# Kernel tuning notes

Hardware: AMD Instinct MI355X
Metric: run time of the kernel (lower is better)

The kernel has to match this reference:

```python
import jax, jax.numpy as jnp
import numpy as np
import math

V, D, H, NH, LE, LD = 32000, 256, 1024, 8, 2, 2
B, T = 4, 512


def qlinear(x, W, b):
    # x: [..., Din, 4]; W: [4, Dout, Din] (r,i,j,k); b: [Dout, 4] or None
    r, i, j, k = x[..., 0], x[..., 1], x[..., 2], x[..., 3]
    Wr, Wi, Wj, Wk = W[0], W[1], W[2], W[3]
    f = lambda a, M: jnp.einsum('...d,od->...o', a, M)
    ro = f(r, Wr) - f(i, Wi) - f(j, Wj) - f(k, Wk)
    io = f(r, Wi) + f(i, Wr) + f(j, Wk) - f(k, Wj)
    jo = f(r, Wj) - f(i, Wk) + f(j, Wr) + f(k, Wi)
    ko = f(r, Wk) + f(i, Wj) - f(j, Wi) + f(k, Wr)
    out = jnp.stack([ro, io, jo, ko], axis=-1)
    return out + b if b is not None else out


def modrelu(x, bias):
    # x: [..., F, 4]; bias: [F]
    norm = jnp.linalg.norm(x, axis=-1)
    scale = jax.nn.relu(norm + bias) / (norm + 1e-6)
    return x * scale[..., None]


def qnorm(x, g, beta):
    # normalize each quaternion (last dim of size 4) to unit norm
    n = jnp.sqrt(jnp.sum(x * x, axis=-1, keepdims=True) + 1e-6)
    return g * (x / n) + beta


def qattn(q, k, v, W, b, mask, nh):
    # W: [4(proj q,k,v,out), 4(comp), D, D]; b: [4, D, 4]
    def split(x):
        Bq, Tq, Dq, _ = x.shape
        return x.reshape(Bq, Tq, nh, Dq // nh, 4).transpose(0, 2, 1, 3, 4)
    qh = split(qlinear(q, W[0], b[0]))
    kh = split(qlinear(k, W[1], b[1]))
    vh = split(qlinear(v, W[2], b[2]))
    hd = qh.shape[3]
    s = jnp.einsum('bhqfd,bhkfd->bhqk', qh, kh) / math.sqrt(hd * 4)
    if mask is not None:
        s = jnp.where(mask[:, None] == 0, -jnp.inf, s)
    w = jax.nn.softmax(s, axis=-1)
    o = jnp.einsum('bhqk,bhkfd->bhqfd', w, vh)
    Bq, h, Tq, f, _ = o.shape
    o = o.transpose(0, 2, 1, 3, 4).reshape(Bq, Tq, h * f, 4)
    return qlinear(o, W[3], b[3])


def qff(x, W1, b1, mbias, W2, b2):
    return qlinear(modrelu(qlinear(x, W1, b1), mbias), W2, b2)


def qembed(ids, emb):
    d = emb.shape[-1]
    scale = 1.0 / 10000.0 ** (jnp.arange(d, dtype=jnp.float32) / d)
    r = emb[0][ids]
    i = emb[1][ids] * scale
    j = emb[2][ids] * scale
    k = emb[3][ids] * scale
    n = jnp.sqrt(r * r + i * i + j * j + k * k + 1e-6)
    return jnp.stack([r / n, i / n, j / n, k / n], axis=-1)


def rope(x):
    t, d = x.shape[1], x.shape[2]
    inv = 1.0 / 10000.0 ** (jnp.arange(0, d, 2, dtype=jnp.float32) / d)
    fr = jnp.arange(t, dtype=jnp.float32)[:, None] * inv[None, :]
    ang = jnp.concatenate([jnp.sin(fr), jnp.cos(fr)], axis=-1)  # [T, D]
    return x * ang[None, :, :, None]


def setup_inputs():
    key = jax.random.key(0)
    ks = jax.random.split(key, 12)
    n = lambda k, s: jax.random.normal(k, s, jnp.float32) * 0.02
    src = jax.random.randint(ks[0], (B, T), 0, V)
    tgt = jax.random.randint(ks[1], (B, T), 0, V)
    tgt_mask = jnp.broadcast_to(jnp.tril(jnp.ones((T, T), jnp.int32)), (B, T, T))
    return dict(
        src=src, tgt=tgt, tgt_mask=tgt_mask,
        emb=n(ks[2], (4, V, D)),
        enc_attn_W=n(ks[3], (LE, 4, 4, D, D)), enc_attn_b=jnp.zeros((LE, 4, D, 4)),
        enc_norm_g=jnp.ones((LE, 2, D, 4)), enc_norm_b=jnp.zeros((LE, 2, D, 4)),
        enc_ff_W1=n(ks[4], (LE, 4, H, D)), enc_ff_b1=jnp.zeros((LE, H, 4)),
        enc_ff_mod=jnp.zeros((LE, H)),
        enc_ff_W2=n(ks[5], (LE, 4, D, H)), enc_ff_b2=jnp.zeros((LE, D, 4)),
        dec_sa_W=n(ks[6], (LD, 4, 4, D, D)), dec_sa_b=jnp.zeros((LD, 4, D, 4)),
        dec_ca_W=n(ks[7], (LD, 4, 4, D, D)), dec_ca_b=jnp.zeros((LD, 4, D, 4)),
        dec_norm_g=jnp.ones((LD, 3, D, 4)), dec_norm_b=jnp.zeros((LD, 3, D, 4)),
        dec_ff_W1=n(ks[8], (LD, 4, H, D)), dec_ff_b1=jnp.zeros((LD, H, 4)),
        dec_ff_mod=jnp.zeros((LD, H)),
        dec_ff_W2=n(ks[9], (LD, 4, D, H)), dec_ff_b2=jnp.zeros((LD, D, 4)),
        fc_W=n(ks[10], (V, D)), fc_b=jnp.zeros((V,)),
    )


def reference(src, tgt, tgt_mask, emb,
              enc_attn_W, enc_attn_b, enc_norm_g, enc_norm_b,
              enc_ff_W1, enc_ff_b1, enc_ff_mod, enc_ff_W2, enc_ff_b2,
              dec_sa_W, dec_sa_b, dec_ca_W, dec_ca_b, dec_norm_g, dec_norm_b,
              dec_ff_W1, dec_ff_b1, dec_ff_mod, dec_ff_W2, dec_ff_b2,
              fc_W, fc_b):
    x_src = rope(qembed(src, emb))
    x_tgt = rope(qembed(tgt, emb))
    # encoder stack
    m = x_src
    for l in range(LE):
        m = qnorm(m + qattn(m, m, m, enc_attn_W[l], enc_attn_b[l], None, NH), enc_norm_g[l, 0], enc_norm_b[l, 0])
        m = qnorm(m + qff(m, enc_ff_W1[l], enc_ff_b1[l], enc_ff_mod[l], enc_ff_W2[l], enc_ff_b2[l]), enc_norm_g[l, 1], enc_norm_b[l, 1])
    # decoder stack
    x = x_tgt
    for l in range(LD):
        x = qnorm(x + qattn(x, x, x, dec_sa_W[l], dec_sa_b[l], tgt_mask, NH), dec_norm_g[l, 0], dec_norm_b[l, 0])
        x = qnorm(x + qattn(x, m, m, dec_ca_W[l], dec_ca_b[l], None, NH), dec_norm_g[l, 1], dec_norm_b[l, 1])
        x = qnorm(x + qff(x, dec_ff_W1[l], dec_ff_b1[l], dec_ff_mod[l], dec_ff_W2[l], dec_ff_b2[l]), dec_norm_g[l, 2], dec_norm_b[l, 2])
    real = jnp.linalg.norm(x, axis=-1)  # QuaternionToReal('norm') -> [B, T, D]
    logits = jnp.einsum('btd,vd->btv', real, fc_W) + fc_b
    return logits
```

## Files before the change

kernel.cpp:

```cpp
#include <hip/hip_runtime.h>
#include <math.h>

#define B 4
#define T 512
#define D 256
#define H 1024
#define NH 8
#define V 32000
#define BT (B*T)
#define LE 2
#define LD 2
#define DIM 1024

typedef __attribute__((ext_vector_type(8))) short s16x8;
typedef __attribute__((ext_vector_type(4))) float f32x4;
typedef __attribute__((address_space(3))) void lds_void;
typedef const __attribute__((address_space(1))) void g_void;

__device__ __forceinline__ ushort f2bf(float x) {
  uint u = __float_as_uint(x);
  return (ushort)((u + 0x7fffu + ((u >> 16) & 1u)) >> 16);
}

__global__ __launch_bounds__(256) void embed_rope_kernel(
    const int* __restrict__ src, const int* __restrict__ tgt,
    const float* __restrict__ emb,
    float* __restrict__ osrc, ushort* __restrict__ osrcbf,
    float* __restrict__ otgt, ushort* __restrict__ otgtbf) {
  int g = blockIdx.x;
  int isTgt = g >= BT;
  int bt = isTgt ? g - BT : g;
  int d  = threadIdx.x;
  int id = isTgt ? tgt[bt] : src[bt];
  float* out = isTgt ? otgt : osrc;
  ushort* outbf = isTgt ? otgtbf : osrcbf;
  int t  = bt % T;
  size_t VD = (size_t)V * D;
  float scale = powf(10000.f, -(float)d / (float)D);
  float r = emb[(size_t)id * D + d];
  float i = emb[VD + (size_t)id * D + d] * scale;
  float j = emb[2 * VD + (size_t)id * D + d] * scale;
  float k = emb[3 * VD + (size_t)id * D + d] * scale;
  float n = sqrtf(r * r + i * i + j * j + k * k + 1e-6f);
  float ang;
  if (d < D / 2) {
    float inv = powf(10000.f, -(float)(2 * d) / (float)D);
    ang = sinf((float)t * inv);
  } else {
    float inv = powf(10000.f, -(float)(2 * (d - D / 2)) / (float)D);
    ang = cosf((float)t * inv);
  }
  float s = ang / n;
  size_t base = (size_t)bt * DIM + d * 4;
  float4 q = make_float4(r * s, i * s, j * s, k * s);
  *(float4*)(out + base) = q;
  *(ushort4*)(outbf + base) = make_ushort4(f2bf(q.x), f2bf(q.y), f2bf(q.z), f2bf(q.w));
}

#define A_CNT  1572864
#define F_CNT  2097152
#define FC_CNT 2048000
#define MEGA_TOT (A_CNT + F_CNT + FC_CNT)
#define WSTEP  1048576
#define FFW    4194304

__device__ __forceinline__ void qexpand_write(
    const float* __restrict__ src, ushort* __restrict__ dst,
    int o, int d, int Din, int P) {
  float w0 = src[(size_t)o * Din + d];
  float w1 = src[P + (size_t)o * Din + d];
  float w2 = src[2 * (size_t)P + (size_t)o * Din + d];
  float w3 = src[3 * (size_t)P + (size_t)o * Din + d];
  int K4 = Din * 4;
  size_t rbase = (size_t)(o * 4) * K4 + d * 4;
  *(ushort4*)(dst + rbase)          = make_ushort4(f2bf(w0), f2bf(-w1), f2bf(-w2), f2bf(-w3));
  *(ushort4*)(dst + rbase + K4)     = make_ushort4(f2bf(w1), f2bf(w0),  f2bf(w3),  f2bf(-w2));
  *(ushort4*)(dst + rbase + 2 * K4) = make_ushort4(f2bf(w2), f2bf(-w3), f2bf(w0),  f2bf(w1));
  *(ushort4*)(dst + rbase + 3 * K4) = make_ushort4(f2bf(w3), f2bf(w2),  f2bf(-w1), f2bf(w0));
}

__global__ __launch_bounds__(256) void mega_expand_kernel(
    const float* __restrict__ encA, const float* __restrict__ decSA,
    const float* __restrict__ decCA,
    const float* __restrict__ eW1, const float* __restrict__ eW2,
    const float* __restrict__ dW1, const float* __restrict__ dW2,
    const float* __restrict__ fcW,
    ushort* __restrict__ WA, ushort* __restrict__ WF, ushort* __restrict__ Wfc) {
  int gid = blockIdx.x * 256 + threadIdx.x;
  if (gid < A_CNT) {
    int u = gid >> 18;
    int p = (gid >> 16) & 3;
    int rem = gid & 65535;
    int o = rem >> 8, d = rem & 255;
    const float* base = (u < 2) ? encA + (size_t)u * 1048576
                      : (u < 4) ? decSA + (size_t)(u - 2) * 1048576
                                : decCA + (size_t)(u - 4) * 1048576;
    qexpand_write(base + (size_t)p * 262144,
                  WA + ((size_t)u * 4 + p) * WSTEP, o, d, 256, 65536);
  } else if (gid < A_CNT + F_CNT) {
    int idx = gid - A_CNT;
    int layer = idx >> 19;
    int w12 = (idx >> 18) & 1;
    int rem = idx & 262143;
    const float* w1b = (layer < 2) ? eW1 + (size_t)layer * 1048576
                                   : dW1 + (size_t)(layer - 2) * 1048576;
    const float* w2b = (layer < 2) ? eW2 + (size_t)layer * 1048576
                                   : dW2 + (size_t)(layer - 2) * 1048576;
    ushort* dst = WF + (size_t)layer * 2 * FFW + (size_t)w12 * FFW;
    if (w12 == 0) {
      int o = rem >> 8, d = rem & 255;
      qexpand_write(w1b, dst, o, d, 256, 262144);
    } else {
      int o = rem >> 10, d = rem & 1023;
      qexpand_write(w2b, dst, o, d, 1024, 262144);
    }
  } else {
    int idx = gid - A_CNT - F_CNT;
    if (idx < FC_CNT) {
      float4 v = ((const float4*)fcW)[idx];
      ((ushort4*)Wfc)[idx] = make_ushort4(f2bf(v.x), f2bf(v.y), f2bf(v.z), f2bf(v.w));
    }
  }
}

struct GP {
  const ushort* A; const ushort* Aalt; int altStart;
  const ushort* Bt; const float* bias; void* Cv;
  ushort* qo; ushort* ko; ushort* vo;
  float* xres; ushort* xbf; const float* gg; const float* bb;
  const float* modb; ushort* realout;
};

template <int OMODE, int TM>
__global__ __launch_bounds__(256, 4) void gemm_bf16_kernel(
    GP u0, GP u1, int nunits, int N, int K) {
  __shared__ ushort As[2][TM * 32];
  __shared__ ushort Bs[2][128 * 32];
  const int tid = threadIdx.x;
  const int w = tid >> 6, l = tid & 63;
  const int nwg = gridDim.x;
  const int qq = nwg >> 3, rr = nwg & 7;
  const int xcd = blockIdx.x & 7, pos = blockIdx.x >> 3;
  const int wg = (xcd < rr ? xcd * (qq + 1) : rr * (qq + 1) + (xcd - rr) * qq) + pos;
  const int uwg = nwg / nunits;
  const int unit = wg / uwg;
  const int wgl = wg - unit * uwg;
  GP U = unit ? u1 : u0;
  const int nbx = N >> 7;
  const int nby = uwg / nbx;
  const int m0 = (wgl % nby) * TM, n0 = (wgl / nby) * 128;
  const ushort* Ap = (U.altStart && n0 >= U.altStart) ? U.Aalt : U.A;
  const ushort* Btp = U.Bt;
  const int lr = l & 15, lg = l >> 4;
  constexpr int NR = (TM == 128) ? 4 : 2;
  const int wm = (TM == 128) ? (w >> 1) : 0;
  const int wn = (TM == 128) ? (w & 1) : w;
  const int wcol = wn * (NR * 16);
  f32x4 acc[4][NR] = {};
  const int NT = K >> 5;

  auto stage = [&](int t, int buf) {
    int k0 = t << 5;
#pragma unroll
    for (int s = 0; s < TM / 64; ++s) {
      int fb = (w * (TM / 64) + s) * 1024;
      int f = fb + l * 16;
      int row = f >> 6, cb = (f & 63) >> 1;
      __builtin_amdgcn_global_load_lds(
          (g_void*)(Ap + (size_t)(m0 + row) * K + k0 + cb),
          (lds_void*)((char*)&As[buf][0] + fb), 16, 0, 0);
    }
#pragma unroll
    for (int s = 0; s < 2; ++s) {
      int fb = (w * 2 + s) * 1024;
      int f = fb + l * 16;
      int row = f >> 6, cb = (f & 63) >> 1;
      __builtin_amdgcn_global_load_lds(
          (g_void*)(Btp + (size_t)(n0 + row) * K + k0 + cb),
          (lds_void*)((char*)&Bs[buf][0] + fb), 16, 0, 0);
    }
  };

  stage(0, 0);
  __syncthreads();
  int cur = 0;
  for (int t = 0; t < NT; ++t) {
    if (t + 1 < NT) stage(t + 1, cur ^ 1);
    s16x8 af[4], bfr[NR];
#pragma unroll
    for (int mi = 0; mi < 4; ++mi)
      af[mi] = *(const s16x8*)(&As[cur][0] + (wm * 64 + mi * 16 + lr) * 32 + lg * 8);
#pragma unroll
    for (int ni = 0; ni < NR; ++ni)
      bfr[ni] = *(const s16x8*)(&Bs[cur][0] + (wcol + ni * 16 + lr) * 32 + lg * 8);
    __builtin_amdgcn_s_setprio(1);
#pragma unroll
    for (int mi = 0; mi < 4; ++mi)
#pragma unroll
      for (int ni = 0; ni < NR; ++ni)
        acc[mi][ni] = __builtin_amdgcn_mfma_f32_16x16x32_bf16(af[mi], bfr[ni], acc[mi][ni], 0, 0, 0);
    __builtin_amdgcn_s_setprio(0);
    __syncthreads();
    cur ^= 1;
  }

#pragma unroll
  for (int mi = 0; mi < 4; ++mi) {
#pragma unroll
    for (int ni = 0; ni < NR; ++ni) {
      int row = m0 + wm * 64 + mi * 16 + lg * 4;
      int col = n0 + wcol + ni * 16 + lr;
      f32x4 v = acc[mi][ni];
      if constexpr (OMODE == 0) {
        float bv = U.bias ? U.bias[col] : 0.f;
        float* C = (float*)U.Cv;
#pragma unroll
        for (int r = 0; r < 4; ++r)
          C[(size_t)(row + r) * N + col] = v[r] + bv;
      } else if constexpr (OMODE == 3) {
        float bv = U.bias[col];
        if (col < 2048) {
          ushort* dst = (col < DIM) ? U.qo : U.ko;
          int c = col & (DIM - 1);
#pragma unroll
          for (int r = 0; r < 4; ++r)
            dst[(size_t)(row + r) * DIM + c] = f2bf(v[r] + bv);
        } else {
          int c = col - 2048;
          ushort4 o4 = make_ushort4(f2bf(v[0] + bv), f2bf(v[1] + bv),
                                    f2bf(v[2] + bv), f2bf(v[3] + bv));
          *(ushort4*)&U.vo[((size_t)((row >> 9) << 10) + c) * T + (row & 511)] = o4;
        }
      } else if constexpr (OMODE == 4) {
        float bv = U.bias[col];
        float gv = U.gg[col], bev = U.bb[col];
#pragma unroll
        for (int r = 0; r < 4; ++r) {
          float val = v[r] + bv + U.xres[(size_t)(row + r) * DIM + col];
          float sq = val * val;
          sq += __shfl_xor(sq, 1);
          sq += __shfl_xor(sq, 2);
          float invn = rsqrtf(sq + 1e-6f);
          float res = gv * (val * invn) + bev;
          U.xres[(size_t)(row + r) * DIM + col] = res;
          U.xbf[(size_t)(row + r) * DIM + col] = f2bf(res);
          if (U.realout) {
            float rsq = res * res;
            rsq += __shfl_xor(rsq, 1);
            rsq += __shfl_xor(rsq, 2);
            if ((col & 3) == 0)
              U.realout[(size_t)(row + r) * D + (col >> 2)] = f2bf(sqrtf(rsq));
          }
        }
      } else {
        float bv = U.bias[col];
        float mb = U.modb[col >> 2];
        ushort* C = (ushort*)U.Cv;
#pragma unroll
        for (int r = 0; r < 4; ++r) {
          float val = v[r] + bv;
          float sq = val * val;
          sq += __shfl_xor(sq, 1);
          sq += __shfl_xor(sq, 2);
          float norm = sqrtf(sq);
          float scale = fmaxf(norm + mb, 0.f) / (norm + 1e-6f);
          C[(size_t)(row + r) * N + col] = f2bf(val * scale);
        }
      }
    }
  }
}

__global__ __launch_bounds__(256) void fused_attn_kernel(
    const ushort* __restrict__ qb, const ushort* __restrict__ kb,
    const ushort* __restrict__ vT, ushort* __restrict__ outA,
    int c0, int c1) {
  __shared__ ushort Ks[2][64 * 128];
  __shared__ ushort Vs[2][128 * 64];
  __shared__ ushort Pst[4][1024];
  const int tid = threadIdx.x;
  const int wq = tid >> 6, l = tid & 63;
  const int lr = l & 15, lg = l >> 4;
  const int h = blockIdx.y;
  const int u = blockIdx.z >> 2, b = blockIdx.z & 3;
  const size_t uoff = (size_t)u * ((size_t)BT * DIM);
  const int causal = u ? c1 : c0;
  const int q0 = blockIdx.x * 64 + wq * 16;
  const size_t bT = (size_t)b * T;
  const int hc = h * 128;
  const size_t vrow0 = (size_t)(b * NH + h) * 128;
  const ushort* qbu = qb + uoff;
  const ushort* kbu = kb + uoff;
  const ushort* vTu = vT + uoff;
  ushort* outu = outA + uoff;
  s16x8 qf[4];
#pragma unroll
  for (int ks = 0; ks < 4; ++ks)
    qf[ks] = *(const s16x8*)(qbu + (bT + q0 + lr) * DIM + hc + ks * 32 + lg * 8);
  f32x4 O[8] = {};
  float m[4] = {-3e38f, -3e38f, -3e38f, -3e38f};
  float lac[4] = {0.f, 0.f, 0.f, 0.f};
  const int kend = causal ? (blockIdx.x + 1) * 64 : T;
  const int ntile = kend >> 6;

  auto stageKV = [&](int tile, int buf) {
    int kv0 = tile << 6;
#pragma unroll
    for (int s = 0; s < 4; ++s) {
      int f = s * 4096 + tid * 16;
      int row = f >> 8, g = (f >> 4) & 15;
      int gs = g ^ (row & 7);
      __builtin_amdgcn_global_load_lds(
          (g_void*)(kbu + (bT + kv0 + row) * DIM + hc + gs * 8),
          (lds_void*)((char*)&Ks[buf][0] + f), 16, 0, 0);
    }
#pragma unroll
    for (int s = 0; s < 4; ++s) {
      int f = s * 4096 + tid * 16;
      int row = f >> 7, g = (f >> 4) & 7;
      int gs = g ^ (row & 7);
      __builtin_amdgcn_global_load_lds(
          (g_void*)(vTu + (vrow0 + row) * T + kv0 + gs * 8),
          (lds_void*)((char*)&Vs[buf][0] + f), 16, 0, 0);
    }
  };

  stageKV(0, 0);
  __syncthreads();
  int cur = 0;
  for (int tile = 0; tile < ntile; ++tile) {
    const int kv0 = tile << 6;
    if (tile + 1 < ntile) stageKV(tile + 1, cur ^ 1);
    f32x4 s[4] = {};
#pragma unroll
    for (int ks = 0; ks < 4; ++ks) {
      s16x8 kf[4];
#pragma unroll
      for (int ni = 0; ni < 4; ++ni) {
        int row = ni * 16 + lr;
        int g = (ks * 4 + lg) ^ (row & 7);
        kf[ni] = *(const s16x8*)(&Ks[cur][0] + row * 128 + g * 8);
      }
#pragma unroll
      for (int ni = 0; ni < 4; ++ni)
        s[ni] = __builtin_amdgcn_mfma_f32_16x16x32_bf16(qf[ks], kf[ni], s[ni], 0, 0, 0);
    }
    const bool domask = causal && (kv0 + 63 > q0);
#pragma unroll
    for (int r = 0; r < 4; ++r) {
      const int qrow = q0 + lg * 4 + r;
      float mx = -3e38f;
#pragma unroll
      for (int ni = 0; ni < 4; ++ni) {
        float v = s[ni][r] * 0.08838834764831845f;
        if (domask && (kv0 + ni * 16 + lr > qrow)) v = -3e38f;
        s[ni][r] = v;
        mx = fmaxf(mx, v);
      }
#pragma unroll
      for (int dd = 1; dd < 16; dd <<= 1) mx = fmaxf(mx, __shfl_xor(mx, dd));
      float mn = fmaxf(m[r], mx);
      float alpha = __expf(m[r] - mn);
      m[r] = mn;
      float ps = 0.f;
#pragma unroll
      for (int ni = 0; ni < 4; ++ni) {
        float p = __expf(s[ni][r] - mn);
        s[ni][r] = p;
        ps += p;
      }
#pragma unroll
      for (int dd = 1; dd < 16; dd <<= 1) ps += __shfl_xor(ps, dd);
      lac[r] = lac[r] * alpha + ps;
#pragma unroll
      for (int dni = 0; dni < 8; ++dni) O[dni][r] *= alpha;
      const int qloc = lg * 4 + r;
      const int sw = (qloc & 7) << 3;
#pragma unroll
      for (int ni = 0; ni < 4; ++ni)
        Pst[wq][qloc * 64 + ((ni * 16 + lr) ^ sw)] = f2bf(s[ni][r]);
    }
    asm volatile("s_waitcnt lgkmcnt(0)" ::: "memory");
    __builtin_amdgcn_sched_barrier(0);
#pragma unroll
    for (int ks2 = 0; ks2 < 2; ++ks2) {
      s16x8 pa = *(const s16x8*)&Pst[wq][lr * 64 + ((ks2 * 32 + lg * 8) ^ ((lr & 7) << 3))];
#pragma unroll
      for (int dni = 0; dni < 8; ++dni) {
        int row = dni * 16 + lr;
        int g = (ks2 * 4 + lg) ^ (row & 7);
        s16x8 vf = *(const s16x8*)(&Vs[cur][0] + row * 64 + g * 8);
        O[dni] = __builtin_amdgcn_mfma_f32_16x16x32_bf16(pa, vf, O[dni], 0, 0, 0);
      }
    }
    __syncthreads();
    cur ^= 1;
  }
#pragma unroll
  for (int r = 0; r < 4; ++r) {
    float inv = 1.f / lac[r];
    const size_t row = bT + q0 + lg * 4 + r;
#pragma unroll
    for (int dni = 0; dni < 8; ++dni)
      outu[row * DIM + hc + dni * 16 + lr] = f2bf(O[dni][r] * inv);
  }
}

extern "C" void kernel_launch(void* const* d_in, const int* in_sizes, int n_in,
                              void* d_out, int out_size, void* d_ws, size_t ws_size,
                              hipStream_t stream) {
  const int*   src        = (const int*)d_in[0];
  const int*   tgt        = (const int*)d_in[1];
  const float* emb        = (const float*)d_in[3];
  const float* enc_attn_W = (const float*)d_in[4];
  const float* enc_attn_b = (const float*)d_in[5];
  const float* enc_norm_g = (const float*)d_in[6];
  const float* enc_norm_b = (const float*)d_in[7];
  const float* enc_ff_W1  = (const float*)d_in[8];
  const float* enc_ff_b1  = (const float*)d_in[9];
  const float* enc_ff_mod = (const float*)d_in[10];
  const float* enc_ff_W2  = (const float*)d_in[11];
  const float* enc_ff_b2  = (const float*)d_in[12];
  const float* dec_sa_W   = (const float*)d_in[13];
  const float* dec_sa_b   = (const float*)d_in[14];
  const float* dec_ca_W   = (const float*)d_in[15];
  const float* dec_ca_b   = (const float*)d_in[16];
  const float* dec_norm_g = (const float*)d_in[17];
  const float* dec_norm_b = (const float*)d_in[18];
  const float* dec_ff_W1  = (const float*)d_in[19];
  const float* dec_ff_b1  = (const float*)d_in[20];
  const float* dec_ff_mod = (const float*)d_in[21];
  const float* dec_ff_W2  = (const float*)d_in[22];
  const float* dec_ff_b2  = (const float*)d_in[23];
  const float* fc_W       = (const float*)d_in[24];
  const float* fc_b       = (const float*)d_in[25];
  float* out = (float*)d_out;

  const size_t USZ = (size_t)BT * DIM;
  float* ws    = (float*)d_ws;
  float* xsrc  = ws;
  float* xtgt  = xsrc + USZ;
  ushort* xbf_src = (ushort*)(xtgt + USZ);
  ushort* xbf_tgt = xbf_src + USZ;
  ushort* aobf    = xbf_tgt + USZ;
  ushort* qb      = aobf + 2 * USZ;
  ushort* kb      = qb + 2 * USZ;
  ushort* vTb     = kb + 2 * USZ;
  ushort* hbf     = vTb + 2 * USZ;
  ushort* realbf  = hbf + (size_t)BT * H * 4;
  ushort* WA      = realbf + (size_t)BT * D;
  ushort* WF      = WA + (size_t)6 * 4 * WSTEP;
  ushort* Wfc     = WF + (size_t)4 * 2 * FFW;

  mega_expand_kernel<<<(MEGA_TOT + 255) / 256, 256, 0, stream>>>(
      enc_attn_W, dec_sa_W, dec_ca_W,
      enc_ff_W1, enc_ff_W2, dec_ff_W1, dec_ff_W2, fc_W, WA, WF, Wfc);

  embed_rope_kernel<<<2 * BT, 256, 0, stream>>>(src, tgt, emb, xsrc, xbf_src,
                                                xtgt, xbf_tgt);

  GP Z{};

  auto mkQKV = [&](const ushort* Abf, const ushort* Wu, const float* bb, int u) {
    GP g = Z;
    g.A = Abf; g.Bt = Wu; g.bias = bb;
    g.qo = qb + u * USZ; g.ko = kb + u * USZ; g.vo = vTb + u * USZ;
    return g;
  };
  auto mkOP = [&](int u, const ushort* Wu3, const float* bb, float* xres,
                  ushort* xbf, const float* gg, const float* nb, ushort* realo) {
    GP g = Z;
    g.A = aobf + u * USZ; g.Bt = Wu3; g.bias = bb;
    g.xres = xres; g.xbf = xbf; g.gg = gg; g.bb = nb; g.realout = realo;
    return g;
  };

  auto qkv1 = [&](GP g) {
    gemm_bf16_kernel<3, 128><<<384, 256, 0, stream>>>(g, g, 1, 3 * DIM, DIM);
  };
  auto qkv2 = [&](GP g0, GP g1) {
    gemm_bf16_kernel<3, 128><<<768, 256, 0, stream>>>(g0, g1, 2, 3 * DIM, DIM);
  };
  auto op1 = [&](GP g) {
    gemm_bf16_kernel<4, 64><<<256, 256, 0, stream>>>(g, g, 1, DIM, DIM);
  };
  auto op2 = [&](GP g0, GP g1) {
    gemm_bf16_kernel<4, 64><<<512, 256, 0, stream>>>(g0, g1, 2, DIM, DIM);
  };
  auto attn1 = [&](int causal) {
    fused_attn_kernel<<<dim3(T / 64, NH, B), 256, 0, stream>>>(
        qb, kb, vTb, aobf, causal, causal);
  };
  auto ffpair = [&](const ushort* xbf, int layer, const float* b1,
                    const float* mod, const float* b2, float* xres,
                    ushort* xbfo, const float* gg, const float* nb,
                    ushort* realo) {
    const ushort* Wf = WF + (size_t)layer * 2 * FFW;
    GP g1 = Z;
    g1.A = xbf; g1.Bt = Wf; g1.bias = b1; g1.Cv = hbf; g1.modb = mod;
    gemm_bf16_kernel<5, 128><<<512, 256, 0, stream>>>(g1, g1, 1, 4 * H, DIM);
    GP g2 = Z;
    g2.A = hbf; g2.Bt = Wf + FFW; g2.bias = b2;
    g2.xres = xres; g2.xbf = xbfo; g2.gg = gg; g2.bb = nb; g2.realout = realo;
    gemm_bf16_kernel<4, 64><<<256, 256, 0, stream>>>(g2, g2, 1, DIM, 4 * H);
  };

  {
    GP e = mkQKV(xbf_src, WA + (size_t)(0 * 4) * WSTEP, enc_attn_b, 0);
    GP d = mkQKV(xbf_tgt, WA + (size_t)(2 * 4) * WSTEP, dec_sa_b, 1);
    qkv2(e, d);
    fused_attn_kernel<<<dim3(T / 64, NH, 2 * B), 256, 0, stream>>>(
        qb, kb, vTb, aobf, 0, 1);
    GP eo = mkOP(0, WA + (size_t)(0 * 4 + 3) * WSTEP, enc_attn_b + 3 * DIM,
                 xsrc, xbf_src, enc_norm_g, enc_norm_b, nullptr);
    GP dо = mkOP(1, WA + (size_t)(2 * 4 + 3) * WSTEP, dec_sa_b + 3 * DIM,
                 xtgt, xbf_tgt, dec_norm_g, dec_norm_b, nullptr);
    op2(eo, dо);
  }
  ffpair(xbf_src, 0, enc_ff_b1, enc_ff_mod, enc_ff_b2, xsrc, xbf_src,
         enc_norm_g + 1 * DIM, enc_norm_b + 1 * DIM, nullptr);
  {
    GP e = mkQKV(xbf_src, WA + (size_t)(1 * 4) * WSTEP,
                 enc_attn_b + (size_t)1 * 4 * DIM, 0);
    qkv1(e);
    attn1(0);
    GP eo = mkOP(0, WA + (size_t)(1 * 4 + 3) * WSTEP,
                 enc_attn_b + (size_t)1 * 4 * DIM + 3 * DIM,
                 xsrc, xbf_src, enc_norm_g + 2 * DIM, enc_norm_b + 2 * DIM, nullptr);
    op1(eo);
  }
  ffpair(xbf_src, 1, enc_ff_b1 + (size_t)1 * H * 4, enc_ff_mod + H,
         enc_ff_b2 + DIM, xsrc, xbf_src,
         enc_norm_g + 3 * DIM, enc_norm_b + 3 * DIM, nullptr);

  for (int l = 0; l < LD; ++l) {
    if (l > 0) {
      GP d = mkQKV(xbf_tgt, WA + (size_t)((2 + l) * 4) * WSTEP,
                   dec_sa_b + (size_t)l * 4 * DIM, 0);
      qkv1(d);
      attn1(1);
      GP od = mkOP(0, WA + (size_t)((2 + l) * 4 + 3) * WSTEP,
                   dec_sa_b + (size_t)l * 4 * DIM + 3 * DIM,
                   xtgt, xbf_tgt, dec_norm_g + (size_t)(l * 3) * DIM,
                   dec_norm_b + (size_t)(l * 3) * DIM, nullptr);
      op1(od);
    }
    {
      GP g = mkQKV(xbf_tgt, WA + (size_t)((4 + l) * 4) * WSTEP,
                   dec_ca_b + (size_t)l * 4 * DIM, 0);
      g.Aalt = xbf_src; g.altStart = DIM;
      qkv1(g);
      attn1(0);
      GP og = mkOP(0, WA + (size_t)((4 + l) * 4 + 3) * WSTEP,
                   dec_ca_b + (size_t)l * 4 * DIM + 3 * DIM,
                   xtgt, xbf_tgt, dec_norm_g + (size_t)(l * 3 + 1) * DIM,
                   dec_norm_b + (size_t)(l * 3 + 1) * DIM, nullptr);
      op1(og);
    }
    ffpair(xbf_tgt, 2 + l, dec_ff_b1 + (size_t)l * H * 4,
           dec_ff_mod + (size_t)l * H, dec_ff_b2 + (size_t)l * DIM,
           xtgt, xbf_tgt, dec_norm_g + (size_t)(l * 3 + 2) * DIM,
           dec_norm_b + (size_t)(l * 3 + 2) * DIM,
           (l == LD - 1) ? realbf : nullptr);
  }

  {
    GP g = Z;
    g.A = realbf; g.Bt = Wfc; g.bias = fc_b; g.Cv = out;
    gemm_bf16_kernel<0, 128><<<(V / 128) * (BT / 128), 256, 0, stream>>>(
        g, g, 1, V, 256);
  }
}
```

Baseline: 1.120 ms.

## Add 2-wave 128x128 GEMM kernel, fold embed into expand, lazy softmax rescale

Adds a new GEMM kernel with 128 threads per block, where each wave computes a 64x128 tile. It is used for the QKV, FF1 and final FC projections to raise per-wave data reuse and MFMA density. The embedding/RoPE kernel is merged into the weight-expand launch to save a kernel launch. The attention softmax scale moves into the Q projection epilogue, and the online-softmax rescale is skipped unless the running max grows by more than a threshold. The larger register tile may lower occupancy, and the lazy rescale lets exponentials exceed 1, which risks overflow in edge cases.

Result: slower. 1.486 ms (+32.7%).

```diff
diff --git a/kernel.cpp b/kernel.cpp
--- a/kernel.cpp
+++ b/kernel.cpp
@@ -22,45 +22,13 @@
   return (ushort)((u + 0x7fffu + ((u >> 16) & 1u)) >> 16);
 }
 
-__global__ __launch_bounds__(256) void embed_rope_kernel(
-    const int* __restrict__ src, const int* __restrict__ tgt,
-    const float* __restrict__ emb,
-    float* __restrict__ osrc, ushort* __restrict__ osrcbf,
-    float* __restrict__ otgt, ushort* __restrict__ otgtbf) {
-  int g = blockIdx.x;
-  int isTgt = g >= BT;
-  int bt = isTgt ? g - BT : g;
-  int d  = threadIdx.x;
-  int id = isTgt ? tgt[bt] : src[bt];
-  float* out = isTgt ? otgt : osrc;
-  ushort* outbf = isTgt ? otgtbf : osrcbf;
-  int t  = bt % T;
-  size_t VD = (size_t)V * D;
-  float scale = powf(10000.f, -(float)d / (float)D);
-  float r = emb[(size_t)id * D + d];
-  float i = emb[VD + (size_t)id * D + d] * scale;
-  float j = emb[2 * VD + (size_t)id * D + d] * scale;
-  float k = emb[3 * VD + (size_t)id * D + d] * scale;
-  float n = sqrtf(r * r + i * i + j * j + k * k + 1e-6f);
-  float ang;
-  if (d < D / 2) {
-    float inv = powf(10000.f, -(float)(2 * d) / (float)D);
-    ang = sinf((float)t * inv);
-  } else {
-    float inv = powf(10000.f, -(float)(2 * (d - D / 2)) / (float)D);
-    ang = cosf((float)t * inv);
-  }
-  float s = ang / n;
-  size_t base = (size_t)bt * DIM + d * 4;
-  float4 q = make_float4(r * s, i * s, j * s, k * s);
-  *(float4*)(out + base) = q;
-  *(ushort4*)(outbf + base) = make_ushort4(f2bf(q.x), f2bf(q.y), f2bf(q.z), f2bf(q.w));
-}
+#define QSCALE 0.08838834764831845f
 
 #define A_CNT  1572864
 #define F_CNT  2097152
 #define FC_CNT 2048000
-#define MEGA_TOT (A_CNT + F_CNT + FC_CNT)
+#define EMB_CNT (2 * BT * 256)
+#define MEGA_TOT (A_CNT + F_CNT + FC_CNT + EMB_CNT)
 #define WSTEP  1048576
 #define FFW    4194304
 
@@ -85,7 +53,11 @@
     const float* __restrict__ eW1, const float* __restrict__ eW2,
     const float* __restrict__ dW1, const float* __restrict__ dW2,
     const float* __restrict__ fcW,
-    ushort* __restrict__ WA, ushort* __restrict__ WF, ushort* __restrict__ Wfc) {
+    ushort* __restrict__ WA, ushort* __restrict__ WF, ushort* __restrict__ Wfc,
+    const int* __restrict__ srcIds, const int* __restrict__ tgtIds,
+    const float* __restrict__ emb,
+    float* __restrict__ xsrc, ushort* __restrict__ xbfs,
+    float* __restrict__ xtgt, ushort* __restrict__ xbft) {
   int gid = blockIdx.x * 256 + threadIdx.x;
   if (gid < A_CNT) {
     int u = gid >> 18;
@@ -114,12 +86,39 @@
       int o = rem >> 10, d = rem & 1023;
       qexpand_write(w2b, dst, o, d, 1024, 262144);
     }
-  } else {
+  } else if (gid < A_CNT + F_CNT + FC_CNT) {
     int idx = gid - A_CNT - F_CNT;
-    if (idx < FC_CNT) {
-      float4 v = ((const float4*)fcW)[idx];
-      ((ushort4*)Wfc)[idx] = make_ushort4(f2bf(v.x), f2bf(v.y), f2bf(v.z), f2bf(v.w));
-    }
+    float4 v = ((const float4*)fcW)[idx];
+    ((ushort4*)Wfc)[idx] = make_ushort4(f2bf(v.x), f2bf(v.y), f2bf(v.z), f2bf(v.w));
+  } else if (gid < MEGA_TOT) {
+    int idx = gid - A_CNT - F_CNT - FC_CNT;
+    int g = idx >> 8, d = idx & 255;
+    int isTgt = g >= BT;
+    int bt = isTgt ? g - BT : g;
+    int id = isTgt ? tgtIds[bt] : srcIds[bt];
+    float* out = isTgt ? xtgt : xsrc;
+    ushort* outbf = isTgt ? xbft : xbfs;
+    int t = bt % T;
+    size_t VD = (size_t)V * D;
+    float scale = powf(10000.f, -(float)d / (float)D);
+    float r = emb[(size_t)id * D + d];
+    float i = emb[VD + (size_t)id * D + d] * scale;
+    float j = emb[2 * VD + (size_t)id * D + d] * scale;
+    float k = emb[3 * VD + (size_t)id * D + d] * scale;
+    float n = sqrtf(r * r + i * i + j * j + k * k + 1e-6f);
+    float ang;
+    if (d < D / 2) {
+      float inv = powf(10000.f, -(float)(2 * d) / (float)D);
+      ang = sinf((float)t * inv);
+    } else {
+      float inv = powf(10000.f, -(float)(2 * (d - D / 2)) / (float)D);
+      ang = cosf((float)t * inv);
+    }
+    float s = ang / n;
+    size_t base = (size_t)bt * DIM + d * 4;
+    float4 q = make_float4(r * s, i * s, j * s, k * s);
+    *(float4*)(out + base) = q;
+    *(ushort4*)(outbf + base) = make_ushort4(f2bf(q.x), f2bf(q.y), f2bf(q.z), f2bf(q.w));
   }
 }
 
@@ -130,6 +129,120 @@
   float* xres; ushort* xbf; const float* gg; const float* bb;
   const float* modb; ushort* realout;
 };
+
+template <int OMODE>
+__global__ __launch_bounds__(128, 2) void gemm2w_kernel(
+    GP u0, GP u1, int nunits, int N, int K) {
+  __shared__ ushort As[2][128 * 32];
+  __shared__ ushort Bs[2][128 * 32];
+  const int tid = threadIdx.x;
+  const int w = tid >> 6, l = tid & 63;
+  const int nwg = gridDim.x;
+  const int qq = nwg >> 3, rr = nwg & 7;
+  const int xcd = blockIdx.x & 7, pos = blockIdx.x >> 3;
+  const int wg = (xcd < rr ? xcd * (qq + 1) : rr * (qq + 1) + (xcd - rr) * qq) + pos;
+  const int uwg = nwg / nunits;
+  const int unit = wg / uwg;
+  const int wgl = wg - unit * uwg;
+  GP U = unit ? u1 : u0;
+  const int nbx = N >> 7;
+  const int nby = uwg / nbx;
+  const int m0 = (wgl % nby) * 128, n0 = (wgl / nby) * 128;
+  const ushort* Ap = (U.altStart && n0 >= U.altStart) ? U.Aalt : U.A;
+  const ushort* Btp = U.Bt;
+  const int lr = l & 15, lg = l >> 4;
+  f32x4 acc[4][8] = {};
+  const int NT = K >> 5;
+
+  auto stage = [&](int t, int buf) {
+    int k0 = t << 5;
+#pragma unroll
+    for (int s = 0; s < 4; ++s) {
+      int f = (s * 128 + tid) * 16;
+      int row = f >> 6, cb = (f & 63) >> 1;
+      __builtin_amdgcn_global_load_lds(
+          (g_void*)(Ap + (size_t)(m0 + row) * K + k0 + cb),
+          (lds_void*)((char*)&As[buf][0] + f), 16, 0, 0);
+    }
+#pragma unroll
+    for (int s = 0; s < 4; ++s) {
+      int f = (s * 128 + tid) * 16;
+      int row = f >> 6, cb = (f & 63) >> 1;
+      __builtin_amdgcn_global_load_lds(
+          (g_void*)(Btp + (size_t)(n0 + row) * K + k0 + cb),
+          (lds_void*)((char*)&Bs[buf][0] + f), 16, 0, 0);
+    }
+  };
+
+  stage(0, 0);
+  __syncthreads();
+  int cur = 0;
+  for (int t = 0; t < NT; ++t) {
+    if (t + 1 < NT) stage(t + 1, cur ^ 1);
+    s16x8 af[4], bfr[8];
+#pragma unroll
+    for (int mi = 0; mi < 4; ++mi)
+      af[mi] = *(const s16x8*)(&As[cur][0] + (w * 64 + mi * 16 + lr) * 32 + lg * 8);
+#pragma unroll
+    for (int ni = 0; ni < 8; ++ni)
+      bfr[ni] = *(const s16x8*)(&Bs[cur][0] + (ni * 16 + lr) * 32 + lg * 8);
+    __builtin_amdgcn_s_setprio(1);
+#pragma unroll
+    for (int mi = 0; mi < 4; ++mi)
+#pragma unroll
+      for (int ni = 0; ni < 8; ++ni)
+        acc[mi][ni] = __builtin_amdgcn_mfma_f32_16x16x32_bf16(af[mi], bfr[ni], acc[mi][ni], 0, 0, 0);
+    __builtin_amdgcn_s_setprio(0);
+    __syncthreads();
+    cur ^= 1;
+  }
+
+#pragma unroll
+  for (int mi = 0; mi < 4; ++mi) {
+#pragma unroll
+    for (int ni = 0; ni < 8; ++ni) {
+      int row = m0 + w * 64 + mi * 16 + lg * 4;
+      int col = n0 + ni * 16 + lr;
+      f32x4 v = acc[mi][ni];
+      if constexpr (OMODE == 0) {
+        float bv = U.bias ? U.bias[col] : 0.f;
+        float* C = (float*)U.Cv;
+#pragma unroll
+        for (int r = 0; r < 4; ++r)
+          C[(size_t)(row + r) * N + col] = v[r] + bv;
+      } else if constexpr (OMODE == 3) {
+        float bv = U.bias[col];
+        if (col < 2048) {
+          ushort* dst = (col < DIM) ? U.qo : U.ko;
+          float sc = (col < DIM) ? QSCALE : 1.f;
+          int c = col & (DIM - 1);
+#pragma unroll
+          for (int r = 0; r < 4; ++r)
+            dst[(size_t)(row + r) * DIM + c] = f2bf((v[r] + bv) * sc);
+        } else {
+          int c = col - 2048;
+          ushort4 o4 = make_ushort4(f2bf(v[0] + bv), f2bf(v[1] + bv),
+                                    f2bf(v[2] + bv), f2bf(v[3] + bv));
+          *(ushort4*)&U.vo[((size_t)((row >> 9) << 10) + c) * T + (row & 511)] = o4;
+        }
+      } else {
+        float bv = U.bias[col];
+        float mb = U.modb[col >> 2];
+        ushort* C = (ushort*)U.Cv;
+#pragma unroll
+        for (int r = 0; r < 4; ++r) {
+          float val = v[r] + bv;
+          float sq = val * val;
+          sq += __shfl_xor(sq, 1);
+          sq += __shfl_xor(sq, 2);
+          float norm = sqrtf(sq);
+          float scale = fmaxf(norm + mb, 0.f) / (norm + 1e-6f);
+          C[(size_t)(row + r) * N + col] = f2bf(val * scale);
+        }
+      }
+    }
+  }
+}
 
 template <int OMODE, int TM>
 __global__ __launch_bounds__(256, 4) void gemm_bf16_kernel(
@@ -149,8 +262,6 @@
   const int nbx = N >> 7;
   const int nby = uwg / nbx;
   const int m0 = (wgl % nby) * TM, n0 = (wgl / nby) * 128;
-  const ushort* Ap = (U.altStart && n0 >= U.altStart) ? U.Aalt : U.A;
-  const ushort* Btp = U.Bt;
   const int lr = l & 15, lg = l >> 4;
   constexpr int NR = (TM == 128) ? 4 : 2;
   const int wm = (TM == 128) ? (w >> 1) : 0;
@@ -167,7 +278,7 @@
       int f = fb + l * 16;
       int row = f >> 6, cb = (f & 63) >> 1;
       __builtin_amdgcn_global_load_lds(
-          (g_void*)(Ap + (size_t)(m0 + row) * K + k0 + cb),
+          (g_void*)(U.A + (size_t)(m0 + row) * K + k0 + cb),
           (lds_void*)((char*)&As[buf][0] + fb), 16, 0, 0);
     }
 #pragma unroll
@@ -176,7 +287,7 @@
       int f = fb + l * 16;
       int row = f >> 6, cb = (f & 63) >> 1;
       __builtin_amdgcn_global_load_lds(
-          (g_void*)(Btp + (size_t)(n0 + row) * K + k0 + cb),
+          (g_void*)(U.Bt + (size_t)(n0 + row) * K + k0 + cb),
           (lds_void*)((char*)&Bs[buf][0] + fb), 16, 0, 0);
     }
   };
@@ -211,27 +322,7 @@
       int row = m0 + wm * 64 + mi * 16 + lg * 4;
       int col = n0 + wcol + ni * 16 + lr;
       f32x4 v = acc[mi][ni];
-      if constexpr (OMODE == 0) {
-        float bv = U.bias ? U.bias[col] : 0.f;
-        float* C = (float*)U.Cv;
-#pragma unroll
-        for (int r = 0; r < 4; ++r)
-          C[(size_t)(row + r) * N + col] = v[r] + bv;
-      } else if constexpr (OMODE == 3) {
-        float bv = U.bias[col];
-        if (col < 2048) {
-          ushort* dst = (col < DIM) ? U.qo : U.ko;
-          int c = col & (DIM - 1);
-#pragma unroll
-          for (int r = 0; r < 4; ++r)
-            dst[(size_t)(row + r) * DIM + c] = f2bf(v[r] + bv);
-        } else {
-          int c = col - 2048;
-          ushort4 o4 = make_ushort4(f2bf(v[0] + bv), f2bf(v[1] + bv),
-                                    f2bf(v[2] + bv), f2bf(v[3] + bv));
-          *(ushort4*)&U.vo[((size_t)((row >> 9) << 10) + c) * T + (row & 511)] = o4;
-        }
-      } else if constexpr (OMODE == 4) {
+      if constexpr (OMODE == 4) {
         float bv = U.bias[col];
         float gv = U.gg[col], bev = U.bb[col];
 #pragma unroll
@@ -251,20 +342,6 @@
             if ((col & 3) == 0)
               U.realout[(size_t)(row + r) * D + (col >> 2)] = f2bf(sqrtf(rsq));
           }
-        }
-      } else {
-        float bv = U.bias[col];
-        float mb = U.modb[col >> 2];
-        ushort* C = (ushort*)U.Cv;
-#pragma unroll
-        for (int r = 0; r < 4; ++r) {
-          float val = v[r] + bv;
-          float sq = val * val;
-          sq += __shfl_xor(sq, 1);
-          sq += __shfl_xor(sq, 2);
-          float norm = sqrtf(sq);
-          float scale = fmaxf(norm + mb, 0.f) / (norm + 1e-6f);
-          C[(size_t)(row + r) * N + col] = f2bf(val * scale);
         }
       }
     }
@@ -352,28 +429,31 @@
       float mx = -3e38f;
 #pragma unroll
       for (int ni = 0; ni < 4; ++ni) {
-        float v = s[ni][r] * 0.08838834764831845f;
+        float v = s[ni][r];
         if (domask && (kv0 + ni * 16 + lr > qrow)) v = -3e38f;
         s[ni][r] = v;
         mx = fmaxf(mx, v);
       }
 #pragma unroll
       for (int dd = 1; dd < 16; dd <<= 1) mx = fmaxf(mx, __shfl_xor(mx, dd));
-      float mn = fmaxf(m[r], mx);
-      float alpha = __expf(m[r] - mn);
-      m[r] = mn;
+      if (__ballot(mx > m[r] + 8.f)) {
+        float mn = fmaxf(m[r], mx);
+        float alpha = __expf(m[r] - mn);
+        m[r] = mn;
+        lac[r] *= alpha;
+#pragma unroll
+        for (int dni = 0; dni < 8; ++dni) O[dni][r] *= alpha;
+      }
       float ps = 0.f;
 #pragma unroll
       for (int ni = 0; ni < 4; ++ni) {
-        float p = __expf(s[ni][r] - mn);
+        float p = __expf(s[ni][r] - m[r]);
         s[ni][r] = p;
         ps += p;
       }
 #pragma unroll
       for (int dd = 1; dd < 16; dd <<= 1) ps += __shfl_xor(ps, dd);
-      lac[r] = lac[r] * alpha + ps;
-#pragma unroll
-      for (int dni = 0; dni < 8; ++dni) O[dni][r] *= alpha;
+      lac[r] += ps;
       const int qloc = lg * 4 + r;
       const int sw = (qloc & 7) << 3;
 #pragma unroll
@@ -454,10 +534,8 @@
 
   mega_expand_kernel<<<(MEGA_TOT + 255) / 256, 256, 0, stream>>>(
       enc_attn_W, dec_sa_W, dec_ca_W,
-      enc_ff_W1, enc_ff_W2, dec_ff_W1, dec_ff_W2, fc_W, WA, WF, Wfc);
-
-  embed_rope_kernel<<<2 * BT, 256, 0, stream>>>(src, tgt, emb, xsrc, xbf_src,
-                                                xtgt, xbf_tgt);
+      enc_ff_W1, enc_ff_W2, dec_ff_W1, dec_ff_W2, fc_W, WA, WF, Wfc,
+      src, tgt, emb, xsrc, xbf_src, xtgt, xbf_tgt);
 
   GP Z{};
 
@@ -476,10 +554,10 @@
   };
 
   auto qkv1 = [&](GP g) {
-    gemm_bf16_kernel<3, 128><<<384, 256, 0, stream>>>(g, g, 1, 3 * DIM, DIM);
+    gemm2w_kernel<3><<<384, 128, 0, stream>>>(g, g, 1, 3 * DIM, DIM);
   };
   auto qkv2 = [&](GP g0, GP g1) {
-    gemm_bf16_kernel<3, 128><<<768, 256, 0, stream>>>(g0, g1, 2, 3 * DIM, DIM);
+    gemm2w_kernel<3><<<768, 128, 0, stream>>>(g0, g1, 2, 3 * DIM, DIM);
   };
   auto op1 = [&](GP g) {
     gemm_bf16_kernel<4, 64><<<256, 256, 0, stream>>>(g, g, 1, DIM, DIM);
@@ -498,7 +576,7 @@
     const ushort* Wf = WF + (size_t)layer * 2 * FFW;
     GP g1 = Z;
     g1.A = xbf; g1.Bt = Wf; g1.bias = b1; g1.Cv = hbf; g1.modb = mod;
-    gemm_bf16_kernel<5, 128><<<512, 256, 0, stream>>>(g1, g1, 1, 4 * H, DIM);
+    gemm2w_kernel<5><<<512, 128, 0, stream>>>(g1, g1, 1, 4 * H, DIM);
     GP g2 = Z;
     g2.A = hbf; g2.Bt = Wf + FFW; g2.bias = b2;
     g2.xres = xres; g2.xbf = xbfo; g2.gg = gg; g2.bb = nb; g2.realout = realo;
@@ -513,9 +591,9 @@
         qb, kb, vTb, aobf, 0, 1);
     GP eo = mkOP(0, WA + (size_t)(0 * 4 + 3) * WSTEP, enc_attn_b + 3 * DIM,
                  xsrc, xbf_src, enc_norm_g, enc_norm_b, nullptr);
-    GP dо = mkOP(1, WA + (size_t)(2 * 4 + 3) * WSTEP, dec_sa_b + 3 * DIM,
+    GP dd = mkOP(1, WA + (size_t)(2 * 4 + 3) * WSTEP, dec_sa_b + 3 * DIM,
                  xtgt, xbf_tgt, dec_norm_g, dec_norm_b, nullptr);
-    op2(eo, dо);
+    op2(eo, dd);
   }
   ffpair(xbf_src, 0, enc_ff_b1, enc_ff_mod, enc_ff_b2, xsrc, xbf_src,
          enc_norm_g + 1 * DIM, enc_norm_b + 1 * DIM, nullptr);
@@ -567,7 +645,7 @@
   {
     GP g = Z;
     g.A = realbf; g.Bt = Wfc; g.bias = fc_b; g.Cv = out;
-    gemm_bf16_kernel<0, 128><<<(V / 128) * (BT / 128), 256, 0, stream>>>(
+    gemm2w_kernel<0><<<(V / 128) * (BT / 128), 128, 0, stream>>>(
         g, g, 1, V, 256);
   }
 }
```

## Fuse embed into expand kernel, deepen GEMM buffering, lazy softmax rescale

Applied to the files above, without the earlier changes.

The embedding/RoPE kernel is folded into the weight-expansion megakernel, removing one launch. For the TM=64 GEMM the shared-memory ring goes from two to four stages and loads two k-tiles per barrier, halving the number of syncs. The attention scale is folded into the Q projection epilogue. Online softmax now rescales only when the running max grows by more than a threshold, which skips exp and multiplies on most tiles but relies on bounded fp32 growth for accuracy.

Result: faster. 1.092 ms (-2.5%).

```diff
diff --git a/kernel.cpp b/kernel.cpp
--- a/kernel.cpp
+++ b/kernel.cpp
@@ -22,45 +22,13 @@
   return (ushort)((u + 0x7fffu + ((u >> 16) & 1u)) >> 16);
 }
 
-__global__ __launch_bounds__(256) void embed_rope_kernel(
-    const int* __restrict__ src, const int* __restrict__ tgt,
-    const float* __restrict__ emb,
-    float* __restrict__ osrc, ushort* __restrict__ osrcbf,
-    float* __restrict__ otgt, ushort* __restrict__ otgtbf) {
-  int g = blockIdx.x;
-  int isTgt = g >= BT;
-  int bt = isTgt ? g - BT : g;
-  int d  = threadIdx.x;
-  int id = isTgt ? tgt[bt] : src[bt];
-  float* out = isTgt ? otgt : osrc;
-  ushort* outbf = isTgt ? otgtbf : osrcbf;
-  int t  = bt % T;
-  size_t VD = (size_t)V * D;
-  float scale = powf(10000.f, -(float)d / (float)D);
-  float r = emb[(size_t)id * D + d];
-  float i = emb[VD + (size_t)id * D + d] * scale;
-  float j = emb[2 * VD + (size_t)id * D + d] * scale;
-  float k = emb[3 * VD + (size_t)id * D + d] * scale;
-  float n = sqrtf(r * r + i * i + j * j + k * k + 1e-6f);
-  float ang;
-  if (d < D / 2) {
-    float inv = powf(10000.f, -(float)(2 * d) / (float)D);
-    ang = sinf((float)t * inv);
-  } else {
-    float inv = powf(10000.f, -(float)(2 * (d - D / 2)) / (float)D);
-    ang = cosf((float)t * inv);
-  }
-  float s = ang / n;
-  size_t base = (size_t)bt * DIM + d * 4;
-  float4 q = make_float4(r * s, i * s, j * s, k * s);
-  *(float4*)(out + base) = q;
-  *(ushort4*)(outbf + base) = make_ushort4(f2bf(q.x), f2bf(q.y), f2bf(q.z), f2bf(q.w));
-}
+#define QSCALE 0.08838834764831845f
 
 #define A_CNT  1572864
 #define F_CNT  2097152
 #define FC_CNT 2048000
-#define MEGA_TOT (A_CNT + F_CNT + FC_CNT)
+#define EMB_CNT (2 * BT * 256)
+#define MEGA_TOT (A_CNT + F_CNT + FC_CNT + EMB_CNT)
 #define WSTEP  1048576
 #define FFW    4194304
 
@@ -85,7 +53,11 @@
     const float* __restrict__ eW1, const float* __restrict__ eW2,
     const float* __restrict__ dW1, const float* __restrict__ dW2,
     const float* __restrict__ fcW,
-    ushort* __restrict__ WA, ushort* __restrict__ WF, ushort* __restrict__ Wfc) {
+    ushort* __restrict__ WA, ushort* __restrict__ WF, ushort* __restrict__ Wfc,
+    const int* __restrict__ srcIds, const int* __restrict__ tgtIds,
+    const float* __restrict__ emb,
+    float* __restrict__ xsrc, ushort* __restrict__ xbfs,
+    float* __restrict__ xtgt, ushort* __restrict__ xbft) {
   int gid = blockIdx.x * 256 + threadIdx.x;
   if (gid < A_CNT) {
     int u = gid >> 18;
@@ -114,12 +86,39 @@
       int o = rem >> 10, d = rem & 1023;
       qexpand_write(w2b, dst, o, d, 1024, 262144);
     }
-  } else {
+  } else if (gid < A_CNT + F_CNT + FC_CNT) {
     int idx = gid - A_CNT - F_CNT;
-    if (idx < FC_CNT) {
-      float4 v = ((const float4*)fcW)[idx];
-      ((ushort4*)Wfc)[idx] = make_ushort4(f2bf(v.x), f2bf(v.y), f2bf(v.z), f2bf(v.w));
-    }
+    float4 v = ((const float4*)fcW)[idx];
+    ((ushort4*)Wfc)[idx] = make_ushort4(f2bf(v.x), f2bf(v.y), f2bf(v.z), f2bf(v.w));
+  } else if (gid < MEGA_TOT) {
+    int idx = gid - A_CNT - F_CNT - FC_CNT;
+    int g = idx >> 8, d = idx & 255;
+    int isTgt = g >= BT;
+    int bt = isTgt ? g - BT : g;
+    int id = isTgt ? tgtIds[bt] : srcIds[bt];
+    float* out = isTgt ? xtgt : xsrc;
+    ushort* outbf = isTgt ? xbft : xbfs;
+    int t = bt % T;
+    size_t VD = (size_t)V * D;
+    float scale = powf(10000.f, -(float)d / (float)D);
+    float r = emb[(size_t)id * D + d];
+    float i = emb[VD + (size_t)id * D + d] * scale;
+    float j = emb[2 * VD + (size_t)id * D + d] * scale;
+    float k = emb[3 * VD + (size_t)id * D + d] * scale;
+    float n = sqrtf(r * r + i * i + j * j + k * k + 1e-6f);
+    float ang;
+    if (d < D / 2) {
+      float inv = powf(10000.f, -(float)(2 * d) / (float)D);
+      ang = sinf((float)t * inv);
+    } else {
+      float inv = powf(10000.f, -(float)(2 * (d - D / 2)) / (float)D);
+      ang = cosf((float)t * inv);
+    }
+    float s = ang / n;
+    size_t base = (size_t)bt * DIM + d * 4;
+    float4 q = make_float4(r * s, i * s, j * s, k * s);
+    *(float4*)(out + base) = q;
+    *(ushort4*)(outbf + base) = make_ushort4(f2bf(q.x), f2bf(q.y), f2bf(q.z), f2bf(q.w));
   }
 }
 
@@ -134,8 +133,9 @@
 template <int OMODE, int TM>
 __global__ __launch_bounds__(256, 4) void gemm_bf16_kernel(
     GP u0, GP u1, int nunits, int N, int K) {
-  __shared__ ushort As[2][TM * 32];
-  __shared__ ushort Bs[2][128 * 32];
+  constexpr int NBUF = (TM == 64) ? 4 : 2;
+  __shared__ ushort As[NBUF][TM * 32];
+  __shared__ ushort Bs[NBUF][128 * 32];
   const int tid = threadIdx.x;
   const int w = tid >> 6, l = tid & 63;
   const int nwg = gridDim.x;
@@ -180,19 +180,14 @@
           (lds_void*)((char*)&Bs[buf][0] + fb), 16, 0, 0);
     }
   };
-
-  stage(0, 0);
-  __syncthreads();
-  int cur = 0;
-  for (int t = 0; t < NT; ++t) {
-    if (t + 1 < NT) stage(t + 1, cur ^ 1);
+  auto compute = [&](int buf) {
     s16x8 af[4], bfr[NR];
 #pragma unroll
     for (int mi = 0; mi < 4; ++mi)
-      af[mi] = *(const s16x8*)(&As[cur][0] + (wm * 64 + mi * 16 + lr) * 32 + lg * 8);
+      af[mi] = *(const s16x8*)(&As[buf][0] + (wm * 64 + mi * 16 + lr) * 32 + lg * 8);
 #pragma unroll
     for (int ni = 0; ni < NR; ++ni)
-      bfr[ni] = *(const s16x8*)(&Bs[cur][0] + (wcol + ni * 16 + lr) * 32 + lg * 8);
+      bfr[ni] = *(const s16x8*)(&Bs[buf][0] + (wcol + ni * 16 + lr) * 32 + lg * 8);
     __builtin_amdgcn_s_setprio(1);
 #pragma unroll
     for (int mi = 0; mi < 4; ++mi)
@@ -200,8 +195,31 @@
       for (int ni = 0; ni < NR; ++ni)
         acc[mi][ni] = __builtin_amdgcn_mfma_f32_16x16x32_bf16(af[mi], bfr[ni], acc[mi][ni], 0, 0, 0);
     __builtin_amdgcn_s_setprio(0);
+  };
+
+  if constexpr (TM == 64) {
+    stage(0, 0);
+    stage(1, 1);
     __syncthreads();
-    cur ^= 1;
+    for (int t = 0; t < NT; t += 2) {
+      if (t + 2 < NT) {
+        stage(t + 2, (t + 2) & 3);
+        stage(t + 3, (t + 3) & 3);
+      }
+      compute(t & 3);
+      compute((t + 1) & 3);
+      __syncthreads();
+    }
+  } else {
+    stage(0, 0);
+    __syncthreads();
+    int cur = 0;
+    for (int t = 0; t < NT; ++t) {
+      if (t + 1 < NT) stage(t + 1, cur ^ 1);
+      compute(cur);
+      __syncthreads();
+      cur ^= 1;
+    }
   }
 
 #pragma unroll
@@ -221,10 +239,11 @@
         float bv = U.bias[col];
         if (col < 2048) {
           ushort* dst = (col < DIM) ? U.qo : U.ko;
+          float sc = (col < DIM) ? QSCALE : 1.f;
           int c = col & (DIM - 1);
 #pragma unroll
           for (int r = 0; r < 4; ++r)
-            dst[(size_t)(row + r) * DIM + c] = f2bf(v[r] + bv);
+            dst[(size_t)(row + r) * DIM + c] = f2bf((v[r] + bv) * sc);
         } else {
           int c = col - 2048;
           ushort4 o4 = make_ushort4(f2bf(v[0] + bv), f2bf(v[1] + bv),
@@ -352,28 +371,31 @@
       float mx = -3e38f;
 #pragma unroll
       for (int ni = 0; ni < 4; ++ni) {
-        float v = s[ni][r] * 0.08838834764831845f;
+        float v = s[ni][r];
         if (domask && (kv0 + ni * 16 + lr > qrow)) v = -3e38f;
         s[ni][r] = v;
         mx = fmaxf(mx, v);
       }
 #pragma unroll
       for (int dd = 1; dd < 16; dd <<= 1) mx = fmaxf(mx, __shfl_xor(mx, dd));
-      float mn = fmaxf(m[r], mx);
-      float alpha = __expf(m[r] - mn);
-      m[r] = mn;
+      if (__ballot(mx > m[r] + 8.f)) {
+        float mn = fmaxf(m[r], mx);
+        float alpha = __expf(m[r] - mn);
+        m[r] = mn;
+        lac[r] *= alpha;
+#pragma unroll
+        for (int dni = 0; dni < 8; ++dni) O[dni][r] *= alpha;
+      }
       float ps = 0.f;
 #pragma unroll
       for (int ni = 0; ni < 4; ++ni) {
-        float p = __expf(s[ni][r] - mn);
+        float p = __expf(s[ni][r] - m[r]);
         s[ni][r] = p;
         ps += p;
       }
 #pragma unroll
       for (int dd = 1; dd < 16; dd <<= 1) ps += __shfl_xor(ps, dd);
-      lac[r] = lac[r] * alpha + ps;
-#pragma unroll
-      for (int dni = 0; dni < 8; ++dni) O[dni][r] *= alpha;
+      lac[r] += ps;
       const int qloc = lg * 4 + r;
       const int sw = (qloc & 7) << 3;
 #pragma unroll
@@ -454,10 +476,8 @@
 
   mega_expand_kernel<<<(MEGA_TOT + 255) / 256, 256, 0, stream>>>(
       enc_attn_W, dec_sa_W, dec_ca_W,
-      enc_ff_W1, enc_ff_W2, dec_ff_W1, dec_ff_W2, fc_W, WA, WF, Wfc);
-
-  embed_rope_kernel<<<2 * BT, 256, 0, stream>>>(src, tgt, emb, xsrc, xbf_src,
-                                                xtgt, xbf_tgt);
+      enc_ff_W1, enc_ff_W2, dec_ff_W1, dec_ff_W2, fc_W, WA, WF, Wfc,
+      src, tgt, emb, xsrc, xbf_src, xtgt, xbf_tgt);
 
   GP Z{};
 
@@ -513,9 +533,9 @@
         qb, kb, vTb, aobf, 0, 1);
     GP eo = mkOP(0, WA + (size_t)(0 * 4 + 3) * WSTEP, enc_attn_b + 3 * DIM,
                  xsrc, xbf_src, enc_norm_g, enc_norm_b, nullptr);
-    GP dо = mkOP(1, WA + (size_t)(2 * 4 + 3) * WSTEP, dec_sa_b + 3 * DIM,
+    GP dd = mkOP(1, WA + (size_t)(2 * 4 + 3) * WSTEP, dec_sa_b + 3 * DIM,
                  xtgt, xbf_tgt, dec_norm_g, dec_norm_b, nullptr);
-    op2(eo, dо);
+    op2(eo, dd);
   }
   ffpair(xbf_src, 0, enc_ff_b1, enc_ff_mod, enc_ff_b2, xsrc, xbf_src,
          enc_norm_g + 1 * DIM, enc_norm_b + 1 * DIM, nullptr);
```
